# Performance work log

Measured on AMD Instinct MI355X. Metric: run time of the kernel, lower is better.

## Reference

```python
import jax, jax.numpy as jnp
import numpy as np
import math

# model / graph sizes
N_NODES, N_EDGES = 50000, 400000
IN_DIM, N_HID = 256, 128
NUM_TYPES, NUM_REL = 4, 5
N_HEADS, D_K = 4, 32
N_LAYERS, MAX_LEN = 2, 240
SQRT_DK = math.sqrt(D_K)


def _gelu(x):
    return jax.nn.gelu(x, approximate=False)  # torch F.gelu is exact erf


def _per_type_linear(x, types, W, b):
    # x:[n,din], types:[n] int, W:[T,din,dout], b:[T,dout]
    out = jnp.zeros((x.shape[0], W.shape[-1]), x.dtype)
    for t in range(W.shape[0]):  # small fixed type count
        out = jnp.where((types == t)[:, None], x @ W[t] + b[t], out)
    return out


def setup_inputs() -> dict:
    key = jax.random.key(0)
    ks = jax.random.split(key, 16)
    node_feature = jax.random.normal(ks[0], (N_NODES, IN_DIM), jnp.float32)
    node_type = jax.random.randint(ks[1], (N_NODES,), 0, NUM_TYPES)
    edge_index = jax.random.randint(ks[2], (2, N_EDGES), 0, N_NODES)
    edge_type = jax.random.randint(ks[3], (N_EDGES,), 0, NUM_REL)
    edge_time = jax.random.randint(ks[4], (N_EDGES,), 0, MAX_LEN)

    def w(k, shape, s=0.05):
        return jax.random.normal(k, shape, jnp.float32) * s

    adapt_W = w(ks[5], (NUM_TYPES, IN_DIM, N_HID))
    adapt_b = jnp.zeros((NUM_TYPES, N_HID), jnp.float32)
    Wk = w(ks[6], (N_LAYERS, NUM_TYPES, N_HID, N_HID))
    Wq = w(ks[7], (N_LAYERS, NUM_TYPES, N_HID, N_HID))
    Wv = w(ks[8], (N_LAYERS, NUM_TYPES, N_HID, N_HID))
    Wa = w(ks[9], (N_LAYERS, NUM_TYPES, N_HID, N_HID))
    bk = jnp.zeros((N_LAYERS, NUM_TYPES, N_HID), jnp.float32)
    bq = jnp.zeros((N_LAYERS, NUM_TYPES, N_HID), jnp.float32)
    bv = jnp.zeros((N_LAYERS, NUM_TYPES, N_HID), jnp.float32)
    ba = jnp.zeros((N_LAYERS, NUM_TYPES, N_HID), jnp.float32)
    rel_pri = jnp.ones((N_LAYERS, NUM_REL, N_HEADS), jnp.float32)
    rel_att = w(ks[10], (N_LAYERS, NUM_REL, N_HEADS, D_K, D_K), 0.1) + jnp.eye(D_K, dtype=jnp.float32)
    rel_msg = w(ks[11], (N_LAYERS, NUM_REL, N_HEADS, D_K, D_K), 0.1) + jnp.eye(D_K, dtype=jnp.float32)
    skip = jnp.ones((N_LAYERS, NUM_TYPES), jnp.float32)
    # fixed sinusoidal RTE table (pyHGT RelTemporalEncoding, requires_grad=False)
    pos = np.arange(MAX_LEN, dtype=np.float32)[:, None]
    div = np.exp(np.arange(0, N_HID, 2, dtype=np.float32) * -(math.log(10000.0) / N_HID))
    tab = np.zeros((MAX_LEN, N_HID), np.float32)
    tab[:, 0::2] = np.sin(pos * div) / math.sqrt(N_HID)
    tab[:, 1::2] = np.cos(pos * div) / math.sqrt(N_HID)
    rte_emb = jnp.asarray(tab)
    rte_W = w(ks[12], (N_LAYERS, N_HID, N_HID))
    rte_b = jnp.zeros((N_LAYERS, N_HID), jnp.float32)
    return dict(node_feature=node_feature, adapt_W=adapt_W, adapt_b=adapt_b,
                Wk=Wk, bk=bk, Wq=Wq, bq=bq, Wv=Wv, bv=bv, Wa=Wa, ba=ba,
                rel_pri=rel_pri, rel_att=rel_att, rel_msg=rel_msg, skip=skip,
                rte_emb=rte_emb, rte_W=rte_W, rte_b=rte_b,
                node_type=node_type, edge_index=edge_index,
                edge_type=edge_type, edge_time=edge_time)


def reference(node_feature, adapt_W, adapt_b, Wk, bk, Wq, bq, Wv, bv, Wa, ba,
              rel_pri, rel_att, rel_msg, skip, rte_emb, rte_W, rte_b,
              node_type, edge_index, edge_type, edge_time):
    n = node_feature.shape[0]
    src, dst = edge_index[0], edge_index[1]  # PyG: row0 = source j, row1 = target i
    st, tt = node_type[src], node_type[dst]
    # per-type input adaptation (all types use Linear + GELU)
    h = _gelu(_per_type_linear(node_feature, node_type, adapt_W, adapt_b))  # [N, n_hid]
    for l in range(N_LAYERS):  # HGTConv stack
        x_j, x_i = h[src], h[dst]
        s_e = x_j + rte_emb[edge_time] @ rte_W[l] + rte_b[l]  # RTE on source per edge
        k = _per_type_linear(s_e, st, Wk[l], bk[l]).reshape(-1, N_HEADS, D_K)
        v = _per_type_linear(s_e, st, Wv[l], bv[l]).reshape(-1, N_HEADS, D_K)
        q = _per_type_linear(x_i, tt, Wq[l], bq[l]).reshape(-1, N_HEADS, D_K)
        att = jnp.zeros((k.shape[0], N_HEADS), h.dtype)
        msg = jnp.zeros_like(v)
        for r in range(NUM_REL):  # small fixed relation count
            m = edge_type == r
            kr = jnp.einsum('ehd,hdk->ehk', k, rel_att[l, r])
            ar = jnp.einsum('ehd,ehd->eh', q, kr) * rel_pri[l, r] / SQRT_DK
            mr = jnp.einsum('ehd,hdk->ehk', v, rel_msg[l, r])
            att = jnp.where(m[:, None], ar, att)
            msg = jnp.where(m[:, None, None], mr, msg)
        # segment softmax over incoming edges of each target node
        amax = jax.lax.stop_gradient(jax.ops.segment_max(att, dst, num_segments=n))
        ex = jnp.exp(att - amax[dst])
        denom = jax.ops.segment_sum(ex, dst, num_segments=n)
        alpha = ex / (denom[dst] + 1e-16)
        aggr = jax.ops.segment_sum((msg * alpha[:, :, None]).reshape(-1, N_HEADS * D_K),
                                   dst, num_segments=n)  # [N, n_hid]
        g = _gelu(aggr)
        res = jnp.zeros_like(h)
        for t in range(NUM_TYPES):  # per-type output transform + gated skip
            a_t = jax.nn.sigmoid(skip[l, t])
            res = jnp.where((node_type == t)[:, None],
                            (g @ Wa[l, t] + ba[l, t]) * a_t + h * (1.0 - a_t), res)
        h = res
    return h
```

## Files before the change

### kernel.cpp

```cpp
#include <hip/hip_runtime.h>
#include <math.h>

#define NN     50000
#define NE     400000
#define INDIM  256
#define NH     128
#define NTYPE  4
#define NREL   5
#define NHEAD  4
#define DK     32
#define RSQRT_DK 0.17677669529663687f
#define BN     64
#define NSCAN_BLK ((NN + 255) / 256)

__device__ __forceinline__ float gelu_f(float x){
    return 0.5f * x * (1.0f + erff(x * 0.70710678118654752f));
}

__global__ void GNN_nscatter(const int* __restrict__ ntype, int* __restrict__ ncur,
                             int* __restrict__ nperm){
    __shared__ int lcnt[4], lbase[4];
    int tid = threadIdx.x;
    if (tid < 4) lcnt[tid] = 0;
    __syncthreads();
    int n = blockIdx.x * 256 + tid;
    int t = 0, lpos = 0;
    bool ok = (n < NN);
    if (ok){ t = ntype[n]; lpos = atomicAdd(&lcnt[t], 1); }
    __syncthreads();
    if (tid < 4 && lcnt[tid] > 0) lbase[tid] = atomicAdd(&ncur[tid], lcnt[tid]);
    __syncthreads();
    if (ok) nperm[t * NN + lbase[t] + lpos] = n;
}

__global__ void GNN_deg(const int* __restrict__ edst, int* __restrict__ deg){
    int e = blockIdx.x * 256 + threadIdx.x;
    if (e < NE) atomicAdd(&deg[edst[e]], 1);
}

__global__ void GNN_scan1(const int* __restrict__ deg, int* __restrict__ rowptr,
                          int* __restrict__ bsum){
    __shared__ int s[256];
    int g = blockIdx.x * 256 + threadIdx.x;
    int v = (g < NN) ? deg[g] : 0;
    s[threadIdx.x] = v;
    __syncthreads();
    for (int off = 1; off < 256; off <<= 1){
        int t = (threadIdx.x >= off) ? s[threadIdx.x - off] : 0;
        __syncthreads();
        s[threadIdx.x] += t;
        __syncthreads();
    }
    if (g < NN) rowptr[g] = s[threadIdx.x] - v;
    if (threadIdx.x == 255) bsum[blockIdx.x] = s[255];
}

__global__ void GNN_scan2(const int* __restrict__ bsum, int* __restrict__ bbase){
    __shared__ int s[256];
    int v = (threadIdx.x < NSCAN_BLK) ? bsum[threadIdx.x] : 0;
    s[threadIdx.x] = v;
    __syncthreads();
    for (int off = 1; off < 256; off <<= 1){
        int t = (threadIdx.x >= off) ? s[threadIdx.x - off] : 0;
        __syncthreads();
        s[threadIdx.x] += t;
        __syncthreads();
    }
    bbase[threadIdx.x] = s[threadIdx.x] - v;
}

__global__ void GNN_scan3(int* __restrict__ rowptr, const int* __restrict__ bbase){
    int g = blockIdx.x * 256 + threadIdx.x;
    if (g < NN) rowptr[g] += bbase[blockIdx.x];
    if (g == 0) rowptr[NN] = NE;
}

__global__ void GNN_csr_scatter(const int* __restrict__ edst, const int* __restrict__ rowptr,
                                int* __restrict__ cursor, int* __restrict__ csr_e){
    int e = blockIdx.x * 256 + threadIdx.x;
    if (e >= NE) return;
    int d = edst[e];
    int pos = atomicAdd(&cursor[d], 1);
    csr_e[rowptr[d] + pos] = e;
}

template<int MODE>
__global__ __launch_bounds__(256) void GNN_ptype_gemm(
    const float* __restrict__ X, int K,
    const float* __restrict__ Wall, const float* __restrict__ ball,
    const float* __restrict__ skiprow, const float* __restrict__ Hprev,
    const int* __restrict__ nperm, const int* __restrict__ counts,
    float* __restrict__ OUT)
{
    int t = blockIdx.y;
    int cnt = counts[t];
    int rbase = blockIdx.x * BN;
    if (rbase >= cnt) return;
    const float* W = Wall + (size_t)t * K * NH;
    __shared__ float Xs[BN][33];
    __shared__ float Ws[32][NH];
    __shared__ int nids[BN];
    int tid = threadIdx.x;
    if (tid < BN){
        int idx = rbase + tid;
        nids[tid] = (idx < cnt) ? nperm[t * NN + idx] : -1;
    }
    int cq = tid & 31;
    int rq = tid >> 5;
    float acc[8][4];
    #pragma unroll
    for (int i = 0; i < 8; i++){ acc[i][0]=0.f; acc[i][1]=0.f; acc[i][2]=0.f; acc[i][3]=0.f; }
    __syncthreads();
    for (int k0 = 0; k0 < K; k0 += 32){
        {
            int lr = tid >> 3;
            int lc = (tid & 7) * 4;
            #pragma unroll
            for (int h2 = 0; h2 < 2; h2++){
                int r = lr + 32 * h2;
                int nid = nids[r];
                float4 xv = make_float4(0.f, 0.f, 0.f, 0.f);
                if (nid >= 0) xv = *(const float4*)(X + (size_t)nid * K + k0 + lc);
                Xs[r][lc+0]=xv.x; Xs[r][lc+1]=xv.y; Xs[r][lc+2]=xv.z; Xs[r][lc+3]=xv.w;
            }
        }
        {
            int wr = tid >> 5;
            int wc = (tid & 31) * 4;
            #pragma unroll
            for (int h2 = 0; h2 < 4; h2++){
                int r = wr + 8 * h2;
                *(float4*)&Ws[r][wc] = *(const float4*)(W + (size_t)(k0 + r) * NH + wc);
            }
        }
        __syncthreads();
        #pragma unroll
        for (int kk = 0; kk < 32; kk++){
            float4 wv = *(const float4*)&Ws[kk][cq * 4];
            #pragma unroll
            for (int i = 0; i < 8; i++){
                float xv = Xs[rq + 8*i][kk];
                acc[i][0] += xv * wv.x; acc[i][1] += xv * wv.y;
                acc[i][2] += xv * wv.z; acc[i][3] += xv * wv.w;
            }
        }
        __syncthreads();
    }
    float b0 = ball[t*NH + cq*4 + 0];
    float b1 = ball[t*NH + cq*4 + 1];
    float b2 = ball[t*NH + cq*4 + 2];
    float b3 = ball[t*NH + cq*4 + 3];
    float a_t = 0.f, one_m = 0.f;
    if (MODE == 2){ a_t = 1.f / (1.f + expf(-skiprow[t])); one_m = 1.f - a_t; }
    #pragma unroll
    for (int i = 0; i < 8; i++){
        int r = rq + 8*i;
        int nid = nids[r];
        if (nid < 0) continue;
        float v0 = acc[i][0] + b0, v1 = acc[i][1] + b1;
        float v2 = acc[i][2] + b2, v3 = acc[i][3] + b3;
        if (MODE == 0){ v0 = gelu_f(v0); v1 = gelu_f(v1); v2 = gelu_f(v2); v3 = gelu_f(v3); }
        if (MODE == 2){
            float4 hp = *(const float4*)(Hprev + (size_t)nid * NH + cq * 4);
            v0 = v0 * a_t + hp.x * one_m; v1 = v1 * a_t + hp.y * one_m;
            v2 = v2 * a_t + hp.z * one_m; v3 = v3 * a_t + hp.w * one_m;
        }
        *(float4*)(OUT + (size_t)nid * NH + cq * 4) = make_float4(v0, v1, v2, v3);
    }
}

__global__ void GNN_rte_tab(const float* __restrict__ rte_emb, const float* __restrict__ rW,
                            const float* __restrict__ rb, float* __restrict__ tab){
    int m = blockIdx.x, j = threadIdx.x;
    __shared__ float e[NH];
    e[j] = rte_emb[m * NH + j];
    __syncthreads();
    float a = rb[j];
    #pragma unroll 8
    for (int d = 0; d < NH; d++) a += e[d] * rW[d * NH + j];
    tab[m * NH + j] = a;
}

__global__ void GNN_rte_proj(const float* __restrict__ tab, const float* __restrict__ WkL,
                             const float* __restrict__ WvL, float* __restrict__ RK,
                             float* __restrict__ RV){
    int m = blockIdx.x, j = threadIdx.x;
    int sel = blockIdx.y; int t = sel >> 1; int which = sel & 1;
    const float* W = (which ? WvL : WkL) + (size_t)t * NH * NH;
    float* O = which ? RV : RK;
    __shared__ float e[NH];
    e[j] = tab[m * NH + j];
    __syncthreads();
    float a = 0.f;
    #pragma unroll 8
    for (int d = 0; d < NH; d++) a += e[d] * W[d * NH + j];
    O[(size_t)(t * 240 + m) * NH + j] = a;
}

__global__ __launch_bounds__(256) void GNN_qa(
    const float* __restrict__ Qn, const float* __restrict__ relA, float* __restrict__ QA)
{
    __shared__ float Atp[4 * 1072];
    __shared__ float Qs[64 * 144];
    int r = blockIdx.y;
    int nb = blockIdx.x * 64;
    int tid = threadIdx.x;
    const float* Ar = relA + (size_t)r * NHEAD * DK * DK;
    for (int x = tid; x < NHEAD * DK * DK; x += 256){
        int hh = x >> 10, rem = x & 1023, dd = rem >> 5, cc = rem & 31;
        Atp[hh * 1072 + (dd >> 2) * 132 + cc * 4 + (dd & 3)] = Ar[x];
    }
    for (int x = tid; x < 64 * 32; x += 256){
        int row = x >> 5, c4w = (x & 31) * 4;
        int hh = c4w >> 5, cc = c4w & 31;
        int node = nb + row;
        float4 qv = make_float4(0.f, 0.f, 0.f, 0.f);
        if (node < NN) qv = *(const float4*)(Qn + (size_t)node * NH + c4w);
        *(float4*)&Qs[row * 144 + hh * 36 + cc] = qv;
    }
    __syncthreads();
    int cq = tid & 31, rq = tid >> 5;
    int h = cq >> 3;
    int abase = h * 1072 + (cq & 7) * 132;
    int qbase = h * 36;
    float acc[8][4];
    #pragma unroll
    for (int i = 0; i < 8; i++){ acc[i][0]=0.f; acc[i][1]=0.f; acc[i][2]=0.f; acc[i][3]=0.f; }
    #pragma unroll 2
    for (int c4 = 0; c4 < 8; c4++){
        float4 av0 = *(const float4*)&Atp[abase + c4 * 16 + 0];
        float4 av1 = *(const float4*)&Atp[abase + c4 * 16 + 4];
        float4 av2 = *(const float4*)&Atp[abase + c4 * 16 + 8];
        float4 av3 = *(const float4*)&Atp[abase + c4 * 16 + 12];
        #pragma unroll
        for (int i = 0; i < 8; i++){
            float4 qv = *(const float4*)&Qs[(rq + 8*i) * 144 + qbase + c4 * 4];
            acc[i][0] += qv.x*av0.x + qv.y*av1.x + qv.z*av2.x + qv.w*av3.x;
            acc[i][1] += qv.x*av0.y + qv.y*av1.y + qv.z*av2.y + qv.w*av3.y;
            acc[i][2] += qv.x*av0.z + qv.y*av1.z + qv.z*av2.z + qv.w*av3.z;
            acc[i][3] += qv.x*av0.w + qv.y*av1.w + qv.z*av2.w + qv.w*av3.w;
        }
    }
    #pragma unroll
    for (int i = 0; i < 8; i++){
        int node = nb + rq + 8*i;
        if (node >= NN) continue;
        *(float4*)(QA + ((size_t)r * NN + node) * NH + cq * 4) =
            make_float4(acc[i][0], acc[i][1], acc[i][2], acc[i][3]);
    }
}

__global__ __launch_bounds__(256) void GNN_edge_att(
    const float* __restrict__ Kn, const float* __restrict__ RK, const float* __restrict__ QA,
    const int* __restrict__ esrc, const int* __restrict__ edst,
    const int* __restrict__ etype, const int* __restrict__ etime,
    const int* __restrict__ ntype, const float* __restrict__ relP,
    float* __restrict__ att)
{
    int tid = threadIdx.x;
    int e = blockIdx.x * 8 + (tid >> 5);
    if (e >= NE) return;
    int lane = tid & 31;
    int s = esrc[e], d = edst[e], r = etype[e], tm = etime[e];
    int st = ntype[s];
    float4 k4 = *(const float4*)(Kn + (size_t)s * NH + lane * 4);
    float4 rk = *(const float4*)(RK + (size_t)(st * 240 + tm) * NH + lane * 4);
    float4 qa = *(const float4*)(QA + ((size_t)r * NN + d) * NH + lane * 4);
    float pv = (k4.x + rk.x) * qa.x + (k4.y + rk.y) * qa.y
             + (k4.z + rk.z) * qa.z + (k4.w + rk.w) * qa.w;
    pv += __shfl_xor(pv, 4);
    pv += __shfl_xor(pv, 2);
    pv += __shfl_xor(pv, 1);
    if ((lane & 7) == 0){
        int head = lane >> 3;
        att[(size_t)e * NHEAD + head] = pv * relP[r * NHEAD + head] * RSQRT_DK;
    }
}

__global__ __launch_bounds__(256) void GNN_node_aggr(
    const float* __restrict__ att, const float* __restrict__ Vn, const float* __restrict__ RV,
    const int* __restrict__ rowptr, const int* __restrict__ csr_e,
    const int* __restrict__ esrc, const int* __restrict__ etype,
    const int* __restrict__ etime, const int* __restrict__ ntype,
    float* __restrict__ P)
{
    int tid = threadIdx.x;
    int i = blockIdx.x * 8 + (tid >> 5);
    if (i >= NN) return;
    int lane = tid & 31;
    int head = lane >> 3;
    int beg = rowptr[i], end = rowptr[i + 1];
    float mx = -3.4e38f;
    for (int k = beg; k < end; k++){
        int e = csr_e[k];
        mx = fmaxf(mx, att[(size_t)e * NHEAD + head]);
    }
    float4 acc[NREL];
    #pragma unroll
    for (int rr = 0; rr < NREL; rr++) acc[rr] = make_float4(0.f, 0.f, 0.f, 0.f);
    float den = 0.f;
    for (int k = beg; k < end; k++){
        int e = csr_e[k];
        int s = esrc[e], r = etype[e], tm = etime[e];
        int st = ntype[s];
        float ex = expf(att[(size_t)e * NHEAD + head] - mx);
        den += ex;
        float4 v4 = *(const float4*)(Vn + (size_t)s * NH + lane * 4);
        float4 rv = *(const float4*)(RV + (size_t)(st * 240 + tm) * NH + lane * 4);
        float vx = v4.x + rv.x, vy = v4.y + rv.y, vz = v4.z + rv.z, vw = v4.w + rv.w;
        #pragma unroll
        for (int rr = 0; rr < NREL; rr++){
            float w = (rr == r) ? ex : 0.f;
            acc[rr].x += w * vx; acc[rr].y += w * vy;
            acc[rr].z += w * vz; acc[rr].w += w * vw;
        }
    }
    float inv = 1.f / (den + 1e-16f);
    #pragma unroll
    for (int rr = 0; rr < NREL; rr++){
        *(float4*)(P + ((size_t)rr * NN + i) * NH + lane * 4) =
            make_float4(acc[rr].x * inv, acc[rr].y * inv, acc[rr].z * inv, acc[rr].w * inv);
    }
}

__global__ __launch_bounds__(256) void GNN_pm(
    const float* __restrict__ P, const float* __restrict__ relM, float* __restrict__ aggr)
{
    __shared__ float Msp[4 * 1072];
    __shared__ float Ps[64 * 144];
    int tid = threadIdx.x;
    int nb = blockIdx.x * 64;
    int cq = tid & 31, rq = tid >> 5;
    int h = cq >> 3;
    int mbase = h * 1072 + (cq & 7) * 132;
    int pbase = h * 36;
    float acc[8][4];
    #pragma unroll
    for (int i = 0; i < 8; i++){ acc[i][0]=0.f; acc[i][1]=0.f; acc[i][2]=0.f; acc[i][3]=0.f; }
    for (int r = 0; r < NREL; r++){
        const float* Mr = relM + (size_t)r * NHEAD * DK * DK;
        for (int x = tid; x < NHEAD * DK * DK; x += 256){
            int hh = x >> 10, rem = x & 1023, dd = rem >> 5, kk = rem & 31;
            Msp[hh * 1072 + (kk >> 2) * 132 + dd * 4 + (kk & 3)] = Mr[x];
        }
        for (int x = tid; x < 64 * 32; x += 256){
            int row = x >> 5, c4w = (x & 31) * 4;
            int hh = c4w >> 5, cc = c4w & 31;
            int node = nb + row;
            float4 pv = make_float4(0.f, 0.f, 0.f, 0.f);
            if (node < NN) pv = *(const float4*)(P + ((size_t)r * NN + node) * NH + c4w);
            *(float4*)&Ps[row * 144 + hh * 36 + cc] = pv;
        }
        __syncthreads();
        #pragma unroll 2
        for (int d4 = 0; d4 < 8; d4++){
            float4 mv0 = *(const float4*)&Msp[mbase + d4 * 16 + 0];
            float4 mv1 = *(const float4*)&Msp[mbase + d4 * 16 + 4];
            float4 mv2 = *(const float4*)&Msp[mbase + d4 * 16 + 8];
            float4 mv3 = *(const float4*)&Msp[mbase + d4 * 16 + 12];
            #pragma unroll
            for (int i = 0; i < 8; i++){
                float4 pv = *(const float4*)&Ps[(rq + 8*i) * 144 + pbase + d4 * 4];
                acc[i][0] += pv.x*mv0.x + pv.y*mv1.x + pv.z*mv2.x + pv.w*mv3.x;
                acc[i][1] += pv.x*mv0.y + pv.y*mv1.y + pv.z*mv2.y + pv.w*mv3.y;
                acc[i][2] += pv.x*mv0.z + pv.y*mv1.z + pv.z*mv2.z + pv.w*mv3.z;
                acc[i][3] += pv.x*mv0.w + pv.y*mv1.w + pv.z*mv2.w + pv.w*mv3.w;
            }
        }
        __syncthreads();
    }
    #pragma unroll
    for (int i = 0; i < 8; i++){
        int node = nb + rq + 8*i;
        if (node >= NN) continue;
        *(float4*)(aggr + (size_t)node * NH + cq * 4) =
            make_float4(gelu_f(acc[i][0]), gelu_f(acc[i][1]),
                        gelu_f(acc[i][2]), gelu_f(acc[i][3]));
    }
}

extern "C" void kernel_launch(void* const* d_in, const int* in_sizes, int n_in,
                              void* d_out, int out_size, void* d_ws, size_t ws_size,
                              hipStream_t stream)
{
    const float* node_feature = (const float*)d_in[0];
    const float* adapt_W = (const float*)d_in[1];
    const float* adapt_b = (const float*)d_in[2];
    const float* Wk = (const float*)d_in[3];
    const float* bk = (const float*)d_in[4];
    const float* Wq = (const float*)d_in[5];
    const float* bq = (const float*)d_in[6];
    const float* Wv = (const float*)d_in[7];
    const float* bv = (const float*)d_in[8];
    const float* Wa = (const float*)d_in[9];
    const float* ba = (const float*)d_in[10];
    const float* rel_pri = (const float*)d_in[11];
    const float* rel_att = (const float*)d_in[12];
    const float* rel_msg = (const float*)d_in[13];
    const float* skip = (const float*)d_in[14];
    const float* rte_emb = (const float*)d_in[15];
    const float* rte_W = (const float*)d_in[16];
    const float* rte_b = (const float*)d_in[17];
    const int* node_type = (const int*)d_in[18];
    const int* edge_index = (const int*)d_in[19];
    const int* edge_type = (const int*)d_in[20];
    const int* edge_time = (const int*)d_in[21];
    const int* esrc = edge_index;
    const int* edst = edge_index + NE;

    char* p = (char*)d_ws;
    auto alloc = [&](size_t bytes) -> char* {
        char* r = p; p += (bytes + 255) & ~(size_t)255; return r;
    };
    float* hA    = (float*)alloc((size_t)NN * NH * 4);
    float* Qn    = (float*)alloc((size_t)NN * NH * 4);
    float* Kn    = (float*)alloc((size_t)NN * NH * 4);
    float* Vn    = (float*)alloc((size_t)NN * NH * 4);
    float* QA    = (float*)alloc((size_t)NREL * NN * NH * 4);
    float* rtab  = (float*)alloc((size_t)240 * NH * 4);
    float* RK    = (float*)alloc((size_t)NTYPE * 240 * NH * 4);
    float* RV    = (float*)alloc((size_t)NTYPE * 240 * NH * 4);
    int* nperm   = (int*)alloc((size_t)NTYPE * NN * 4);
    int* rowptr  = (int*)alloc((size_t)(NN + 1) * 4);
    int* csr_e   = (int*)alloc((size_t)NE * 4);
    int* deg     = (int*)alloc((size_t)2 * NN * 4);
    int* cursor  = deg + NN;
    int* bsum    = (int*)alloc(256 * 4);
    int* bbase   = (int*)alloc(256 * 4);
    int* ncur    = (int*)alloc(64);
    float* att   = Qn;
    float* Pbuf  = QA;
    float* aggr  = Kn;

    hipMemsetAsync(ncur, 0, 64, stream);
    hipMemsetAsync(deg, 0, (size_t)2 * NN * 4, stream);

    GNN_nscatter<<<(NN + 255) / 256, 256, 0, stream>>>(node_type, ncur, nperm);
    GNN_deg<<<(NE + 255) / 256, 256, 0, stream>>>(edst, deg);
    GNN_scan1<<<NSCAN_BLK, 256, 0, stream>>>(deg, rowptr, bsum);
    GNN_scan2<<<1, 256, 0, stream>>>(bsum, bbase);
    GNN_scan3<<<NSCAN_BLK, 256, 0, stream>>>(rowptr, bbase);
    GNN_csr_scatter<<<(NE + 255) / 256, 256, 0, stream>>>(edst, rowptr, cursor, csr_e);

    dim3 ggrid((NN + BN - 1) / BN, NTYPE);
    GNN_ptype_gemm<0><<<ggrid, 256, 0, stream>>>(node_feature, INDIM, adapt_W, adapt_b,
                                                 nullptr, nullptr, nperm, ncur, hA);
    const float* hin = hA;
    for (int l = 0; l < 2; l++){
        const float* WkL = Wk + (size_t)l * NTYPE * NH * NH;
        const float* WqL = Wq + (size_t)l * NTYPE * NH * NH;
        const float* WvL = Wv + (size_t)l * NTYPE * NH * NH;
        const float* WaL = Wa + (size_t)l * NTYPE * NH * NH;
        const float* bkL = bk + (size_t)l * NTYPE * NH;
        const float* bqL = bq + (size_t)l * NTYPE * NH;
        const float* bvL = bv + (size_t)l * NTYPE * NH;
        const float* baL = ba + (size_t)l * NTYPE * NH;
        const float* relA = rel_att + (size_t)l * NREL * NHEAD * DK * DK;
        const float* relM = rel_msg + (size_t)l * NREL * NHEAD * DK * DK;
        const float* relP = rel_pri + (size_t)l * NREL * NHEAD;

        GNN_rte_tab<<<240, 128, 0, stream>>>(rte_emb, rte_W + (size_t)l * NH * NH,
                                             rte_b + (size_t)l * NH, rtab);
        GNN_rte_proj<<<dim3(240, NTYPE * 2), 128, 0, stream>>>(rtab, WkL, WvL, RK, RV);

        GNN_ptype_gemm<1><<<ggrid, 256, 0, stream>>>(hin, NH, WqL, bqL, nullptr, nullptr,
                                                     nperm, ncur, Qn);
        GNN_qa<<<dim3((NN + 63) / 64, NREL), 256, 0, stream>>>(Qn, relA, QA);
        GNN_ptype_gemm<1><<<ggrid, 256, 0, stream>>>(hin, NH, WkL, bkL, nullptr, nullptr,
                                                     nperm, ncur, Kn);
        GNN_ptype_gemm<1><<<ggrid, 256, 0, stream>>>(hin, NH, WvL, bvL, nullptr, nullptr,
                                                     nperm, ncur, Vn);

        GNN_edge_att<<<(NE + 7) / 8, 256, 0, stream>>>(
            Kn, RK, QA, esrc, edst, edge_type, edge_time, node_type, relP, att);

        GNN_node_aggr<<<(NN + 7) / 8, 256, 0, stream>>>(
            att, Vn, RV, rowptr, csr_e, esrc, edge_type, edge_time, node_type, Pbuf);

        GNN_pm<<<(NN + 63) / 64, 256, 0, stream>>>(Pbuf, relM, aggr);

        float* hout = (l == 0) ? hA : (float*)d_out;
        GNN_ptype_gemm<2><<<ggrid, 256, 0, stream>>>(
            aggr, NH, WaL, baL, skip + (size_t)l * NTYPE, hin,
            nperm, ncur, hout);
        hin = hout;
    }
}
```

Measured before the change: 1.219 ms.

## Restructure per-type GEMM with register prefetch and larger per-thread tiles

Rewrites the per-type node GEMM to use 128 threads, each computing an 8x8 output tile split across two column halves. The next K-slice is prefetched from global memory into registers while the current slice is computed, and X is read from shared memory as float4. This is meant to raise arithmetic intensity per shared-memory load and hide global load latency, at the cost of higher register pressure and fewer threads per block.

```diff
diff --git a/kernel.cpp b/kernel.cpp
--- a/kernel.cpp
+++ b/kernel.cpp
@@ -85,7 +85,7 @@
 }
 
 template<int MODE>
-__global__ __launch_bounds__(256) void GNN_ptype_gemm(
+__global__ __launch_bounds__(128) void GNN_ptype_gemm(
     const float* __restrict__ X, int K,
     const float* __restrict__ Wall, const float* __restrict__ ball,
     const float* __restrict__ skiprow, const float* __restrict__ Hprev,
@@ -97,59 +97,87 @@
     int rbase = blockIdx.x * BN;
     if (rbase >= cnt) return;
     const float* W = Wall + (size_t)t * K * NH;
-    __shared__ float Xs[BN][33];
-    __shared__ float Ws[32][NH];
+    __shared__ float Xs[64 * 36];
+    __shared__ float Ws[32 * 128];
     __shared__ int nids[BN];
     int tid = threadIdx.x;
     if (tid < BN){
         int idx = rbase + tid;
         nids[tid] = (idx < cnt) ? nperm[t * NN + idx] : -1;
     }
-    int cq = tid & 31;
-    int rq = tid >> 5;
-    float acc[8][4];
-    #pragma unroll
-    for (int i = 0; i < 8; i++){ acc[i][0]=0.f; acc[i][1]=0.f; acc[i][2]=0.f; acc[i][3]=0.f; }
-    __syncthreads();
+    __syncthreads();
+
+    float4 xr[4], wr[8];
+    auto loadX = [&](int k0){
+        #pragma unroll
+        for (int j = 0; j < 4; j++){
+            int slot = j * 128 + tid;
+            int row = slot >> 3, c4 = slot & 7;
+            int nid = nids[row];
+            xr[j] = make_float4(0.f, 0.f, 0.f, 0.f);
+            if (nid >= 0) xr[j] = *(const float4*)(X + (size_t)nid * K + k0 + c4 * 4);
+        }
+    };
+    auto loadW = [&](int k0){
+        #pragma unroll
+        for (int j = 0; j < 8; j++){
+            int slot = j * 128 + tid;
+            wr[j] = *(const float4*)(W + (size_t)(k0 + (slot >> 5)) * NH + (slot & 31) * 4);
+        }
+    };
+
+    int cq = tid & 15, rq = tid >> 4;
+    float accA[8][4], accB[8][4];
+    #pragma unroll
+    for (int i = 0; i < 8; i++){
+        accA[i][0]=0.f; accA[i][1]=0.f; accA[i][2]=0.f; accA[i][3]=0.f;
+        accB[i][0]=0.f; accB[i][1]=0.f; accB[i][2]=0.f; accB[i][3]=0.f;
+    }
+
+    loadX(0); loadW(0);
     for (int k0 = 0; k0 < K; k0 += 32){
-        {
-            int lr = tid >> 3;
-            int lc = (tid & 7) * 4;
-            #pragma unroll
-            for (int h2 = 0; h2 < 2; h2++){
-                int r = lr + 32 * h2;
-                int nid = nids[r];
-                float4 xv = make_float4(0.f, 0.f, 0.f, 0.f);
-                if (nid >= 0) xv = *(const float4*)(X + (size_t)nid * K + k0 + lc);
-                Xs[r][lc+0]=xv.x; Xs[r][lc+1]=xv.y; Xs[r][lc+2]=xv.z; Xs[r][lc+3]=xv.w;
-            }
-        }
-        {
-            int wr = tid >> 5;
-            int wc = (tid & 31) * 4;
-            #pragma unroll
-            for (int h2 = 0; h2 < 4; h2++){
-                int r = wr + 8 * h2;
-                *(float4*)&Ws[r][wc] = *(const float4*)(W + (size_t)(k0 + r) * NH + wc);
-            }
-        }
-        __syncthreads();
-        #pragma unroll
-        for (int kk = 0; kk < 32; kk++){
-            float4 wv = *(const float4*)&Ws[kk][cq * 4];
+        #pragma unroll
+        for (int j = 0; j < 4; j++){
+            int slot = j * 128 + tid;
+            int row = slot >> 3, c4 = slot & 7;
+            *(float4*)&Xs[row * 36 + c4 * 4] = xr[j];
+        }
+        #pragma unroll
+        for (int j = 0; j < 8; j++){
+            int slot = j * 128 + tid;
+            *(float4*)&Ws[slot * 4] = wr[j];
+        }
+        __syncthreads();
+        if (k0 + 32 < K){ loadX(k0 + 32); loadW(k0 + 32); }
+        #pragma unroll
+        for (int c4 = 0; c4 < 8; c4++){
+            float4 w0A = *(const float4*)&Ws[(c4*4+0)*128 + cq*4];
+            float4 w1A = *(const float4*)&Ws[(c4*4+1)*128 + cq*4];
+            float4 w2A = *(const float4*)&Ws[(c4*4+2)*128 + cq*4];
+            float4 w3A = *(const float4*)&Ws[(c4*4+3)*128 + cq*4];
+            float4 w0B = *(const float4*)&Ws[(c4*4+0)*128 + cq*4 + 64];
+            float4 w1B = *(const float4*)&Ws[(c4*4+1)*128 + cq*4 + 64];
+            float4 w2B = *(const float4*)&Ws[(c4*4+2)*128 + cq*4 + 64];
+            float4 w3B = *(const float4*)&Ws[(c4*4+3)*128 + cq*4 + 64];
             #pragma unroll
             for (int i = 0; i < 8; i++){
-                float xv = Xs[rq + 8*i][kk];
-                acc[i][0] += xv * wv.x; acc[i][1] += xv * wv.y;
-                acc[i][2] += xv * wv.z; acc[i][3] += xv * wv.w;
+                float4 xv = *(const float4*)&Xs[(rq + 8*i) * 36 + c4 * 4];
+                accA[i][0] += xv.x*w0A.x + xv.y*w1A.x + xv.z*w2A.x + xv.w*w3A.x;
+                accA[i][1] += xv.x*w0A.y + xv.y*w1A.y + xv.z*w2A.y + xv.w*w3A.y;
+                accA[i][2] += xv.x*w0A.z + xv.y*w1A.z + xv.z*w2A.z + xv.w*w3A.z;
+                accA[i][3] += xv.x*w0A.w + xv.y*w1A.w + xv.z*w2A.w + xv.w*w3A.w;
+                accB[i][0] += xv.x*w0B.x + xv.y*w1B.x + xv.z*w2B.x + xv.w*w3B.x;
+                accB[i][1] += xv.x*w0B.y + xv.y*w1B.y + xv.z*w2B.y + xv.w*w3B.y;
+                accB[i][2] += xv.x*w0B.z + xv.y*w1B.z + xv.z*w2B.z + xv.w*w3B.z;
+                accB[i][3] += xv.x*w0B.w + xv.y*w1B.w + xv.z*w2B.w + xv.w*w3B.w;
             }
         }
         __syncthreads();
     }
-    float b0 = ball[t*NH + cq*4 + 0];
-    float b1 = ball[t*NH + cq*4 + 1];
-    float b2 = ball[t*NH + cq*4 + 2];
-    float b3 = ball[t*NH + cq*4 + 3];
+
+    int colA = cq * 4, colB = cq * 4 + 64;
+    float4 bA = *(const float4*)(ball + t * NH + colA);
+    float4 bB = *(const float4*)(ball + t * NH + colB);
     float a_t = 0.f, one_m = 0.f;
     if (MODE == 2){ a_t = 1.f / (1.f + expf(-skiprow[t])); one_m = 1.f - a_t; }
     #pragma unroll
@@ -157,15 +185,24 @@
         int r = rq + 8*i;
         int nid = nids[r];
         if (nid < 0) continue;
-        float v0 = acc[i][0] + b0, v1 = acc[i][1] + b1;
-        float v2 = acc[i][2] + b2, v3 = acc[i][3] + b3;
-        if (MODE == 0){ v0 = gelu_f(v0); v1 = gelu_f(v1); v2 = gelu_f(v2); v3 = gelu_f(v3); }
+        float vA0 = accA[i][0] + bA.x, vA1 = accA[i][1] + bA.y;
+        float vA2 = accA[i][2] + bA.z, vA3 = accA[i][3] + bA.w;
+        float vB0 = accB[i][0] + bB.x, vB1 = accB[i][1] + bB.y;
+        float vB2 = accB[i][2] + bB.z, vB3 = accB[i][3] + bB.w;
+        if (MODE == 0){
+            vA0 = gelu_f(vA0); vA1 = gelu_f(vA1); vA2 = gelu_f(vA2); vA3 = gelu_f(vA3);
+            vB0 = gelu_f(vB0); vB1 = gelu_f(vB1); vB2 = gelu_f(vB2); vB3 = gelu_f(vB3);
+        }
         if (MODE == 2){
-            float4 hp = *(const float4*)(Hprev + (size_t)nid * NH + cq * 4);
-            v0 = v0 * a_t + hp.x * one_m; v1 = v1 * a_t + hp.y * one_m;
-            v2 = v2 * a_t + hp.z * one_m; v3 = v3 * a_t + hp.w * one_m;
-        }
-        *(float4*)(OUT + (size_t)nid * NH + cq * 4) = make_float4(v0, v1, v2, v3);
+            float4 hpA = *(const float4*)(Hprev + (size_t)nid * NH + colA);
+            float4 hpB = *(const float4*)(Hprev + (size_t)nid * NH + colB);
+            vA0 = vA0 * a_t + hpA.x * one_m; vA1 = vA1 * a_t + hpA.y * one_m;
+            vA2 = vA2 * a_t + hpA.z * one_m; vA3 = vA3 * a_t + hpA.w * one_m;
+            vB0 = vB0 * a_t + hpB.x * one_m; vB1 = vB1 * a_t + hpB.y * one_m;
+            vB2 = vB2 * a_t + hpB.z * one_m; vB3 = vB3 * a_t + hpB.w * one_m;
+        }
+        *(float4*)(OUT + (size_t)nid * NH + colA) = make_float4(vA0, vA1, vA2, vA3);
+        *(float4*)(OUT + (size_t)nid * NH + colB) = make_float4(vB0, vB1, vB2, vB3);
     }
 }
 
@@ -443,7 +480,7 @@
     GNN_csr_scatter<<<(NE + 255) / 256, 256, 0, stream>>>(edst, rowptr, cursor, csr_e);
 
     dim3 ggrid((NN + BN - 1) / BN, NTYPE);
-    GNN_ptype_gemm<0><<<ggrid, 256, 0, stream>>>(node_feature, INDIM, adapt_W, adapt_b,
+    GNN_ptype_gemm<0><<<ggrid, 128, 0, stream>>>(node_feature, INDIM, adapt_W, adapt_b,
                                                  nullptr, nullptr, nperm, ncur, hA);
     const float* hin = hA;
     for (int l = 0; l < 2; l++){
@@ -463,12 +500,12 @@
                                              rte_b + (size_t)l * NH, rtab);
         GNN_rte_proj<<<dim3(240, NTYPE * 2), 128, 0, stream>>>(rtab, WkL, WvL, RK, RV);
 
-        GNN_ptype_gemm<1><<<ggrid, 256, 0, stream>>>(hin, NH, WqL, bqL, nullptr, nullptr,
+        GNN_ptype_gemm<1><<<ggrid, 128, 0, stream>>>(hin, NH, WqL, bqL, nullptr, nullptr,
                                                      nperm, ncur, Qn);
         GNN_qa<<<dim3((NN + 63) / 64, NREL), 256, 0, stream>>>(Qn, relA, QA);
-        GNN_ptype_gemm<1><<<ggrid, 256, 0, stream>>>(hin, NH, WkL, bkL, nullptr, nullptr,
+        GNN_ptype_gemm<1><<<ggrid, 128, 0, stream>>>(hin, NH, WkL, bkL, nullptr, nullptr,
                                                      nperm, ncur, Kn);
-        GNN_ptype_gemm<1><<<ggrid, 256, 0, stream>>>(hin, NH, WvL, bvL, nullptr, nullptr,
+        GNN_ptype_gemm<1><<<ggrid, 128, 0, stream>>>(hin, NH, WvL, bvL, nullptr, nullptr,
                                                      nperm, ncur, Vn);
 
         GNN_edge_att<<<(NE + 7) / 8, 256, 0, stream>>>(
@@ -480,7 +517,7 @@
         GNN_pm<<<(NN + 63) / 64, 256, 0, stream>>>(Pbuf, relM, aggr);
 
         float* hout = (l == 0) ? hA : (float*)d_out;
-        GNN_ptype_gemm<2><<<ggrid, 256, 0, stream>>>(
+        GNN_ptype_gemm<2><<<ggrid, 128, 0, stream>>>(
             aggr, NH, WaL, baL, skip + (size_t)l * NTYPE, hin,
             nperm, ncur, hout);
         hin = hout;
```

New measurement: 3.384 ms. 2.78x slower.

## Restage GEMM X tile k-major with float4 LDS reads and merge Q/K/V launches

Applied to the files above, without the earlier changes.

Factors the per-type GEMM into a shared device tile routine. The X tile is now stored k-major in groups of four (padded stride 260), so the inner loop reads float4 values of X and four W rows per step instead of scalar X loads. Q, K and V projections are combined into one launch using a z grid dimension, which removes two kernel launches and the tail effects between them. The new packing and larger per-iteration register set could change occupancy or create LDS bank conflicts.

```diff
diff --git a/kernel.cpp b/kernel.cpp
--- a/kernel.cpp
+++ b/kernel.cpp
@@ -12,6 +12,7 @@
 #define RSQRT_DK 0.17677669529663687f
 #define BN     64
 #define NSCAN_BLK ((NN + 255) / 256)
+#define XB     260
 
 __device__ __forceinline__ float gelu_f(float x){
     return 0.5f * x * (1.0f + erff(x * 0.70710678118654752f));
@@ -85,6 +86,75 @@
 }
 
 template<int MODE>
+__device__ __forceinline__ void gemm_tile(
+    const float* __restrict__ X, int K,
+    const float* __restrict__ W, const float* __restrict__ brow,
+    float a_t, const float* __restrict__ Hprev,
+    float* Xs, float* Ws, const int* nids,
+    float* __restrict__ OUT)
+{
+    int tid = threadIdx.x;
+    int cq = tid & 31, rq = tid >> 5;
+    float acc[8][4];
+    #pragma unroll
+    for (int i = 0; i < 8; i++){ acc[i][0]=0.f; acc[i][1]=0.f; acc[i][2]=0.f; acc[i][3]=0.f; }
+
+    for (int k0 = 0; k0 < K; k0 += 32){
+        #pragma unroll
+        for (int j = 0; j < 2; j++){
+            int slot = j * 256 + tid;
+            int c4 = slot >> 6, row = slot & 63;
+            int nid = nids[row];
+            float4 xv = make_float4(0.f, 0.f, 0.f, 0.f);
+            if (nid >= 0) xv = *(const float4*)(X + (size_t)nid * K + k0 + c4 * 4);
+            *(float4*)&Xs[c4 * XB + row * 4] = xv;
+        }
+        #pragma unroll
+        for (int j = 0; j < 4; j++){
+            int slot = j * 256 + tid;
+            int kk = slot >> 5, col4 = slot & 31;
+            *(float4*)&Ws[kk * 128 + col4 * 4] =
+                *(const float4*)(W + (size_t)(k0 + kk) * NH + col4 * 4);
+        }
+        __syncthreads();
+        #pragma unroll 2
+        for (int c4 = 0; c4 < 8; c4++){
+            float4 w0 = *(const float4*)&Ws[(c4*4+0)*128 + cq*4];
+            float4 w1 = *(const float4*)&Ws[(c4*4+1)*128 + cq*4];
+            float4 w2 = *(const float4*)&Ws[(c4*4+2)*128 + cq*4];
+            float4 w3 = *(const float4*)&Ws[(c4*4+3)*128 + cq*4];
+            #pragma unroll
+            for (int i = 0; i < 8; i++){
+                float4 xv = *(const float4*)&Xs[c4 * XB + (rq + 8*i) * 4];
+                acc[i][0] += xv.x*w0.x + xv.y*w1.x + xv.z*w2.x + xv.w*w3.x;
+                acc[i][1] += xv.x*w0.y + xv.y*w1.y + xv.z*w2.y + xv.w*w3.y;
+                acc[i][2] += xv.x*w0.z + xv.y*w1.z + xv.z*w2.z + xv.w*w3.z;
+                acc[i][3] += xv.x*w0.w + xv.y*w1.w + xv.z*w2.w + xv.w*w3.w;
+            }
+        }
+        __syncthreads();
+    }
+
+    float4 b4 = *(const float4*)(brow + cq * 4);
+    float one_m = 1.f - a_t;
+    #pragma unroll
+    for (int i = 0; i < 8; i++){
+        int r = rq + 8*i;
+        int nid = nids[r];
+        if (nid < 0) continue;
+        float v0 = acc[i][0] + b4.x, v1 = acc[i][1] + b4.y;
+        float v2 = acc[i][2] + b4.z, v3 = acc[i][3] + b4.w;
+        if (MODE == 0){ v0 = gelu_f(v0); v1 = gelu_f(v1); v2 = gelu_f(v2); v3 = gelu_f(v3); }
+        if (MODE == 2){
+            float4 hp = *(const float4*)(Hprev + (size_t)nid * NH + cq * 4);
+            v0 = v0 * a_t + hp.x * one_m; v1 = v1 * a_t + hp.y * one_m;
+            v2 = v2 * a_t + hp.z * one_m; v3 = v3 * a_t + hp.w * one_m;
+        }
+        *(float4*)(OUT + (size_t)nid * NH + cq * 4) = make_float4(v0, v1, v2, v3);
+    }
+}
+
+template<int MODE>
 __global__ __launch_bounds__(256) void GNN_ptype_gemm(
     const float* __restrict__ X, int K,
     const float* __restrict__ Wall, const float* __restrict__ ball,
@@ -96,77 +166,48 @@
     int cnt = counts[t];
     int rbase = blockIdx.x * BN;
     if (rbase >= cnt) return;
-    const float* W = Wall + (size_t)t * K * NH;
-    __shared__ float Xs[BN][33];
-    __shared__ float Ws[32][NH];
+    __shared__ float Xs[8 * XB];
+    __shared__ float Ws[32 * 128];
     __shared__ int nids[BN];
     int tid = threadIdx.x;
     if (tid < BN){
         int idx = rbase + tid;
         nids[tid] = (idx < cnt) ? nperm[t * NN + idx] : -1;
     }
-    int cq = tid & 31;
-    int rq = tid >> 5;
-    float acc[8][4];
-    #pragma unroll
-    for (int i = 0; i < 8; i++){ acc[i][0]=0.f; acc[i][1]=0.f; acc[i][2]=0.f; acc[i][3]=0.f; }
-    __syncthreads();
-    for (int k0 = 0; k0 < K; k0 += 32){
-        {
-            int lr = tid >> 3;
-            int lc = (tid & 7) * 4;
-            #pragma unroll
-            for (int h2 = 0; h2 < 2; h2++){
-                int r = lr + 32 * h2;
-                int nid = nids[r];
-                float4 xv = make_float4(0.f, 0.f, 0.f, 0.f);
-                if (nid >= 0) xv = *(const float4*)(X + (size_t)nid * K + k0 + lc);
-                Xs[r][lc+0]=xv.x; Xs[r][lc+1]=xv.y; Xs[r][lc+2]=xv.z; Xs[r][lc+3]=xv.w;
-            }
-        }
-        {
-            int wr = tid >> 5;
-            int wc = (tid & 31) * 4;
-            #pragma unroll
-            for (int h2 = 0; h2 < 4; h2++){
-                int r = wr + 8 * h2;
-                *(float4*)&Ws[r][wc] = *(const float4*)(W + (size_t)(k0 + r) * NH + wc);
-            }
-        }
-        __syncthreads();
-        #pragma unroll
-        for (int kk = 0; kk < 32; kk++){
-            float4 wv = *(const float4*)&Ws[kk][cq * 4];
-            #pragma unroll
-            for (int i = 0; i < 8; i++){
-                float xv = Xs[rq + 8*i][kk];
-                acc[i][0] += xv * wv.x; acc[i][1] += xv * wv.y;
-                acc[i][2] += xv * wv.z; acc[i][3] += xv * wv.w;
-            }
-        }
-        __syncthreads();
-    }
-    float b0 = ball[t*NH + cq*4 + 0];
-    float b1 = ball[t*NH + cq*4 + 1];
-    float b2 = ball[t*NH + cq*4 + 2];
-    float b3 = ball[t*NH + cq*4 + 3];
-    float a_t = 0.f, one_m = 0.f;
-    if (MODE == 2){ a_t = 1.f / (1.f + expf(-skiprow[t])); one_m = 1.f - a_t; }
-    #pragma unroll
-    for (int i = 0; i < 8; i++){
-        int r = rq + 8*i;
-        int nid = nids[r];
-        if (nid < 0) continue;
-        float v0 = acc[i][0] + b0, v1 = acc[i][1] + b1;
-        float v2 = acc[i][2] + b2, v3 = acc[i][3] + b3;
-        if (MODE == 0){ v0 = gelu_f(v0); v1 = gelu_f(v1); v2 = gelu_f(v2); v3 = gelu_f(v3); }
-        if (MODE == 2){
-            float4 hp = *(const float4*)(Hprev + (size_t)nid * NH + cq * 4);
-            v0 = v0 * a_t + hp.x * one_m; v1 = v1 * a_t + hp.y * one_m;
-            v2 = v2 * a_t + hp.z * one_m; v3 = v3 * a_t + hp.w * one_m;
-        }
-        *(float4*)(OUT + (size_t)nid * NH + cq * 4) = make_float4(v0, v1, v2, v3);
-    }
+    __syncthreads();
+    float a_t = 0.f;
+    if (MODE == 2) a_t = 1.f / (1.f + expf(-skiprow[t]));
+    gemm_tile<MODE>(X, K, Wall + (size_t)t * K * NH, ball + t * NH,
+                    a_t, Hprev, Xs, Ws, nids, OUT);
+}
+
+__global__ __launch_bounds__(256) void GNN_qkv_gemm(
+    const float* __restrict__ X,
+    const float* __restrict__ Wq, const float* __restrict__ bq,
+    const float* __restrict__ Wk, const float* __restrict__ bk,
+    const float* __restrict__ Wv, const float* __restrict__ bv,
+    const int* __restrict__ nperm, const int* __restrict__ counts,
+    float* __restrict__ Qn, float* __restrict__ Kn, float* __restrict__ Vn)
+{
+    int t = blockIdx.y;
+    int cnt = counts[t];
+    int rbase = blockIdx.x * BN;
+    if (rbase >= cnt) return;
+    __shared__ float Xs[8 * XB];
+    __shared__ float Ws[32 * 128];
+    __shared__ int nids[BN];
+    int tid = threadIdx.x;
+    if (tid < BN){
+        int idx = rbase + tid;
+        nids[tid] = (idx < cnt) ? nperm[t * NN + idx] : -1;
+    }
+    __syncthreads();
+    int z = blockIdx.z;
+    const float* W = (z == 0) ? Wq : (z == 1) ? Wk : Wv;
+    const float* b = (z == 0) ? bq : (z == 1) ? bk : bv;
+    float* OUT     = (z == 0) ? Qn : (z == 1) ? Kn : Vn;
+    gemm_tile<1>(X, NH, W + (size_t)t * NH * NH, b + t * NH,
+                 0.f, nullptr, Xs, Ws, nids, OUT);
 }
 
 __global__ void GNN_rte_tab(const float* __restrict__ rte_emb, const float* __restrict__ rW,
@@ -463,13 +504,10 @@
                                              rte_b + (size_t)l * NH, rtab);
         GNN_rte_proj<<<dim3(240, NTYPE * 2), 128, 0, stream>>>(rtab, WkL, WvL, RK, RV);
 
-        GNN_ptype_gemm<1><<<ggrid, 256, 0, stream>>>(hin, NH, WqL, bqL, nullptr, nullptr,
-                                                     nperm, ncur, Qn);
+        GNN_qkv_gemm<<<dim3(ggrid.x, NTYPE, 3), 256, 0, stream>>>(
+            hin, WqL, bqL, WkL, bkL, WvL, bvL, nperm, ncur, Qn, Kn, Vn);
+
         GNN_qa<<<dim3((NN + 63) / 64, NREL), 256, 0, stream>>>(Qn, relA, QA);
-        GNN_ptype_gemm<1><<<ggrid, 256, 0, stream>>>(hin, NH, WkL, bkL, nullptr, nullptr,
-                                                     nperm, ncur, Kn);
-        GNN_ptype_gemm<1><<<ggrid, 256, 0, stream>>>(hin, NH, WvL, bvL, nullptr, nullptr,
-                                                     nperm, ncur, Vn);
 
         GNN_edge_att<<<(NE + 7) / 8, 256, 0, stream>>>(
             Kn, RK, QA, esrc, edst, edge_type, edge_time, node_type, relP, att);
```

Result: faster. 1.156 ms (-5.2%).
